# Kernel tuning notes

Hardware: AMD Instinct MI355X
Metric: run time of the kernel (lower is better)

## Reference

```python
import jax, jax.numpy as jnp
import numpy as np

INPUT, HIDDEN, OUTPUT = 512, 512, 512
B, S = 32, 2048


def setup_inputs() -> dict:
    key = jax.random.key(0)
    ks = jax.random.split(key, 8)
    s_in = 1.0 / np.sqrt(INPUT)
    s_h = 1.0 / np.sqrt(HIDDEN)
    return {
        "x": jax.random.normal(ks[0], (B, S, INPUT), dtype=jnp.float32),
        "W_xh": jax.random.uniform(ks[1], (HIDDEN, INPUT), jnp.float32, -s_in, s_in),
        "b_xh": jax.random.uniform(ks[2], (HIDDEN,), jnp.float32, -s_in, s_in),
        "W_hh": jax.random.uniform(ks[3], (HIDDEN, HIDDEN), jnp.float32, -s_h, s_h),
        "b_hh": jax.random.uniform(ks[4], (HIDDEN,), jnp.float32, -s_h, s_h),
        "b_h": jnp.zeros((HIDDEN,), jnp.float32),
        "W_fc": jax.random.uniform(ks[5], (OUTPUT, HIDDEN), jnp.float32, -s_h, s_h),
        "b_fc": jax.random.uniform(ks[6], (OUTPUT,), jnp.float32, -s_h, s_h),
    }


def reference(x, W_xh, b_xh, W_hh, b_hh, b_h, W_fc, b_fc):
    # Precompute the input projection for all timesteps in one big GEMM:
    # [B,S,I] @ [I,H] -> [B,S,H]; bias terms folded in once.
    xproj = jnp.einsum("bsi,hi->bsh", x, W_xh) + (b_xh + b_hh + b_h)
    h0 = jnp.zeros((x.shape[0], W_hh.shape[0]), x.dtype)

    def step(h, xp_t):
        h = jnp.tanh(xp_t + h @ W_hh.T)
        return h, None

    # scan over time: xproj transposed to [S,B,H]
    h_final, _ = jax.lax.scan(step, h0, jnp.swapaxes(xproj, 0, 1))
    return h_final @ W_fc.T + b_fc
```

## Files before the change

### kernel.cpp

```cpp
#include <hip/hip_runtime.h>

typedef _Float16 f16;
typedef _Float16 f16x8 __attribute__((ext_vector_type(8)));
typedef float    f32x4 __attribute__((ext_vector_type(4)));

#define NSTEP 2048
#define HID   512
#define BATCH 32
#define SEQL  2048

__global__ __launch_bounds__(256, 4) void wcvt_kernel(
    const float* __restrict__ W, f16* __restrict__ Wf)
{
    int i = (blockIdx.x * 256 + threadIdx.x) * 8;
    float4 a0 = *(const float4*)(W + i);
    float4 a1 = *(const float4*)(W + i + 4);
    f16x8 h;
    h[0] = (f16)a0.x; h[1] = (f16)a0.y; h[2] = (f16)a0.z; h[3] = (f16)a0.w;
    h[4] = (f16)a1.x; h[5] = (f16)a1.y; h[6] = (f16)a1.z; h[7] = (f16)a1.w;
    *(f16x8*)&Wf[i] = h;
}

#define P1_AS 40

__global__ __launch_bounds__(256, 2) void xproj_f16_kernel(
    const float* __restrict__ x, const f16* __restrict__ Wf16,
    const float* __restrict__ bxh, const float* __restrict__ bhh,
    const float* __restrict__ bh, f16* __restrict__ xp)
{
    __shared__ __align__(16) f16 As[64 * P1_AS];
    __shared__ __align__(16) f16 Bs[512 * P1_AS];

    const int t = threadIdx.x;
    const int wave = t >> 6, lane = t & 63;
    const size_t mbase = (size_t)blockIdx.x * 64;

    f32x4 acc[4][8];
#pragma unroll
    for (int i = 0; i < 4; i++)
#pragma unroll
        for (int j = 0; j < 8; j++) acc[i][j] = (f32x4){0.f, 0.f, 0.f, 0.f};

    const int r_st = t >> 2;
    const int koff = (t & 3) * 8;

    for (int k0 = 0; k0 < 512; k0 += 32) {
        __syncthreads();
        {
            const float* src = x + (mbase + r_st) * 512 + k0 + koff;
            float4 a0 = *(const float4*)src;
            float4 a1 = *(const float4*)(src + 4);
            f16x8 h;
            h[0] = (f16)a0.x; h[1] = (f16)a0.y; h[2] = (f16)a0.z; h[3] = (f16)a0.w;
            h[4] = (f16)a1.x; h[5] = (f16)a1.y; h[6] = (f16)a1.z; h[7] = (f16)a1.w;
            *(f16x8*)&As[r_st * P1_AS + koff] = h;
        }
#pragma unroll
        for (int i = 0; i < 8; i++) {
            int n = r_st + i * 64;
            *(f16x8*)&Bs[n * P1_AS + koff] =
                *(const f16x8*)(Wf16 + (size_t)n * 512 + k0 + koff);
        }
        __syncthreads();

        f16x8 af[4];
#pragma unroll
        for (int rt = 0; rt < 4; rt++)
            af[rt] = *(const f16x8*)&As[(rt * 16 + (lane & 15)) * P1_AS + (lane >> 4) * 8];
#pragma unroll
        for (int ct = 0; ct < 8; ct++) {
            f16x8 bf = *(const f16x8*)&Bs[((wave * 8 + ct) * 16 + (lane & 15)) * P1_AS + (lane >> 4) * 8];
#pragma unroll
            for (int rt = 0; rt < 4; rt++)
                acc[rt][ct] = __builtin_amdgcn_mfma_f32_16x16x32_f16(af[rt], bf, acc[rt][ct], 0, 0, 0);
        }
    }

#pragma unroll
    for (int ct = 0; ct < 8; ct++) {
        int n = wave * 128 + ct * 16 + (lane & 15);
        float bias = bxh[n] + bhh[n] + bh[n];
#pragma unroll
        for (int rt = 0; rt < 4; rt++) {
#pragma unroll
            for (int r = 0; r < 4; r++) {
                size_t m = mbase + rt * 16 + (lane >> 4) * 4 + r;
                xp[m * 512 + n] = (f16)(acc[rt][ct][r] + bias);
            }
        }
    }
}

__global__ __launch_bounds__(256, 2) void xproj_kernel(
    const float* __restrict__ x, const float* __restrict__ Wxh,
    const float* __restrict__ bxh, const float* __restrict__ bhh,
    const float* __restrict__ bh, f16* __restrict__ xp)
{
    __shared__ __align__(16) f16 As[64 * P1_AS];
    __shared__ __align__(16) f16 Bs[512 * P1_AS];

    const int t = threadIdx.x;
    const int wave = t >> 6, lane = t & 63;
    const size_t mbase = (size_t)blockIdx.x * 64;

    f32x4 acc[4][8];
#pragma unroll
    for (int i = 0; i < 4; i++)
#pragma unroll
        for (int j = 0; j < 8; j++) acc[i][j] = (f32x4){0.f, 0.f, 0.f, 0.f};

    const int r_st = t >> 2;
    const int koff = (t & 3) * 8;

    for (int k0 = 0; k0 < 512; k0 += 32) {
        __syncthreads();
        {
            const float* src = x + (mbase + r_st) * 512 + k0 + koff;
            float4 a0 = *(const float4*)src;
            float4 a1 = *(const float4*)(src + 4);
            f16x8 h;
            h[0] = (f16)a0.x; h[1] = (f16)a0.y; h[2] = (f16)a0.z; h[3] = (f16)a0.w;
            h[4] = (f16)a1.x; h[5] = (f16)a1.y; h[6] = (f16)a1.z; h[7] = (f16)a1.w;
            *(f16x8*)&As[r_st * P1_AS + koff] = h;
        }
#pragma unroll
        for (int i = 0; i < 8; i++) {
            int n = r_st + i * 64;
            const float* src = Wxh + (size_t)n * 512 + k0 + koff;
            float4 b0 = *(const float4*)src;
            float4 b1 = *(const float4*)(src + 4);
            f16x8 h;
            h[0] = (f16)b0.x; h[1] = (f16)b0.y; h[2] = (f16)b0.z; h[3] = (f16)b0.w;
            h[4] = (f16)b1.x; h[5] = (f16)b1.y; h[6] = (f16)b1.z; h[7] = (f16)b1.w;
            *(f16x8*)&Bs[n * P1_AS + koff] = h;
        }
        __syncthreads();

        f16x8 af[4];
#pragma unroll
        for (int rt = 0; rt < 4; rt++)
            af[rt] = *(const f16x8*)&As[(rt * 16 + (lane & 15)) * P1_AS + (lane >> 4) * 8];
#pragma unroll
        for (int ct = 0; ct < 8; ct++) {
            f16x8 bf = *(const f16x8*)&Bs[((wave * 8 + ct) * 16 + (lane & 15)) * P1_AS + (lane >> 4) * 8];
#pragma unroll
            for (int rt = 0; rt < 4; rt++)
                acc[rt][ct] = __builtin_amdgcn_mfma_f32_16x16x32_f16(af[rt], bf, acc[rt][ct], 0, 0, 0);
        }
    }

#pragma unroll
    for (int ct = 0; ct < 8; ct++) {
        int n = wave * 128 + ct * 16 + (lane & 15);
        float bias = bxh[n] + bhh[n] + bh[n];
#pragma unroll
        for (int rt = 0; rt < 4; rt++) {
#pragma unroll
            for (int r = 0; r < 4; r++) {
                size_t m = mbase + rt * 16 + (lane >> 4) * 4 + r;
                xp[m * 512 + n] = (f16)(acc[rt][ct][r] + bias);
            }
        }
    }
}

#define P2_LDS_BYTES (2 * HID * 2 + 8 * 16 * 64 * 16)

__global__ __launch_bounds__(512, 2) void rnn_kernel(
    const float* __restrict__ Whh, const f16* __restrict__ xp,
    f16* __restrict__ hfin)
{
    extern __shared__ __align__(16) char smem[];
    f16* hbuf0 = (f16*)smem;
    f16* hbuf1 = hbuf0 + HID;
    f16* ldsB  = hbuf1 + HID;

    const int t = threadIdx.x;
    const int wave = t >> 6, lane = t & 63;
    const int b = blockIdx.x;

    const int c_in = lane & 15;
    const int k8   = (lane >> 4) * 8;

    f16x8 wreg[48];
#pragma unroll
    for (int r = 0; r < 3; r++) {
        const float* wrow = Whh + (size_t)((wave * 4 + r) * 16 + c_in) * 512;
#pragma unroll
        for (int kf = 0; kf < 16; kf++) {
            float4 w0 = *(const float4*)(wrow + kf * 32 + k8);
            float4 w1 = *(const float4*)(wrow + kf * 32 + k8 + 4);
            f16x8 h;
            h[0] = (f16)w0.x; h[1] = (f16)w0.y; h[2] = (f16)w0.z; h[3] = (f16)w0.w;
            h[4] = (f16)w1.x; h[5] = (f16)w1.y; h[6] = (f16)w1.z; h[7] = (f16)w1.w;
            wreg[r * 16 + kf] = h;
        }
    }
    {
        const float* wrow = Whh + (size_t)((wave * 4 + 3) * 16 + c_in) * 512;
#pragma unroll
        for (int kf = 0; kf < 16; kf++) {
            float4 w0 = *(const float4*)(wrow + kf * 32 + k8);
            float4 w1 = *(const float4*)(wrow + kf * 32 + k8 + 4);
            f16x8 h;
            h[0] = (f16)w0.x; h[1] = (f16)w0.y; h[2] = (f16)w0.z; h[3] = (f16)w0.w;
            h[4] = (f16)w1.x; h[5] = (f16)w1.y; h[6] = (f16)w1.z; h[7] = (f16)w1.w;
            *(f16x8*)&ldsB[(size_t)wave * 8192 + kf * 512 + lane * 8] = h;
        }
    }
    hbuf0[t & (HID - 1)] = (f16)0.f;
    __syncthreads();

    const f16* xprow = xp + (size_t)b * SEQL * 512 + wave * 64 + lane;
    const int ldsb_base = wave * 8192 + lane * 8;

    float xv = (float)xprow[0];
    for (int s = 0; s < NSTEP; s++) {
        const f16* cur = (s & 1) ? hbuf1 : hbuf0;
        f16*       nxt = (s & 1) ? hbuf0 : hbuf1;
        int sn = (s + 1 < NSTEP) ? s + 1 : s;
        float xv_next = (float)xprow[(size_t)sn * 512];

        f32x4 a0 = (f32x4){0.f,0.f,0.f,0.f}, a1 = a0, a2 = a0, a3 = a0;
#pragma unroll
        for (int kf = 0; kf < 16; kf++) {
            f16x8 av = *(const f16x8*)&cur[kf * 32 + k8];
            a0 = __builtin_amdgcn_mfma_f32_16x16x32_f16(av, wreg[kf],      a0, 0, 0, 0);
            a1 = __builtin_amdgcn_mfma_f32_16x16x32_f16(av, wreg[16 + kf], a1, 0, 0, 0);
            a2 = __builtin_amdgcn_mfma_f32_16x16x32_f16(av, wreg[32 + kf], a2, 0, 0, 0);
            f16x8 bl = *(const f16x8*)&ldsB[ldsb_base + kf * 512];
            a3 = __builtin_amdgcn_mfma_f32_16x16x32_f16(av, bl, a3, 0, 0, 0);
        }
        int r = lane >> 4;
        float v = (r == 0) ? a0[0] : (r == 1) ? a1[0] : (r == 2) ? a2[0] : a3[0];
        v += xv;
        float e = __expf(2.f * v);
        v = 1.f - 2.f / (e + 1.f);
        nxt[wave * 64 + lane] = (f16)v;
        xv = xv_next;
        __syncthreads();
    }
    hfin[(size_t)b * 512 + t] = hbuf0[t & (HID - 1)];
}

#define P3_HS 520

__global__ __launch_bounds__(256, 2) void fc_kernel(
    const f16* __restrict__ hfin, const float* __restrict__ Wfc,
    const float* __restrict__ bfc, float* __restrict__ out)
{
    __shared__ __align__(16) f16 hs[BATCH * P3_HS];
    const int t = threadIdx.x;
    for (int i = 0; i < 64; i++) {
        int e = i * 256 + t;
        hs[(e >> 9) * P3_HS + (e & 511)] = hfin[e];
    }
    __syncthreads();

    const int bidx = t & 31;
    const int oi = t >> 5;
    const int o0 = blockIdx.x * 16;
    const int oA = o0 + oi, oB = o0 + oi + 8;
    const float* wA = Wfc + (size_t)oA * 512;
    const float* wB = Wfc + (size_t)oB * 512;

    float sA = 0.f, sB = 0.f;
#pragma unroll 4
    for (int kb = 0; kb < 64; kb++) {
        f16x8 hv = *(const f16x8*)&hs[bidx * P3_HS + kb * 8];
        float4 wa0 = *(const float4*)(wA + kb * 8);
        float4 wa1 = *(const float4*)(wA + kb * 8 + 4);
        float4 wb0 = *(const float4*)(wB + kb * 8);
        float4 wb1 = *(const float4*)(wB + kb * 8 + 4);
        float h0 = (float)hv[0], h1 = (float)hv[1], h2 = (float)hv[2], h3 = (float)hv[3];
        float h4 = (float)hv[4], h5 = (float)hv[5], h6 = (float)hv[6], h7 = (float)hv[7];
        sA += wa0.x*h0 + wa0.y*h1 + wa0.z*h2 + wa0.w*h3 + wa1.x*h4 + wa1.y*h5 + wa1.z*h6 + wa1.w*h7;
        sB += wb0.x*h0 + wb0.y*h1 + wb0.z*h2 + wb0.w*h3 + wb1.x*h4 + wb1.y*h5 + wb1.z*h6 + wb1.w*h7;
    }
    out[(size_t)bidx * 512 + oA] = sA + bfc[oA];
    out[(size_t)bidx * 512 + oB] = sB + bfc[oB];
}

extern "C" void kernel_launch(void* const* d_in, const int* in_sizes, int n_in,
                              void* d_out, int out_size, void* d_ws, size_t ws_size,
                              hipStream_t stream) {
    const float* x    = (const float*)d_in[0];
    const float* Wxh  = (const float*)d_in[1];
    const float* bxh  = (const float*)d_in[2];
    const float* Whh  = (const float*)d_in[3];
    const float* bhh  = (const float*)d_in[4];
    const float* bh   = (const float*)d_in[5];
    const float* Wfc  = (const float*)d_in[6];
    const float* bfc  = (const float*)d_in[7];
    float* outp = (float*)d_out;

    const size_t xp_bytes   = (size_t)BATCH * SEQL * 512 * 2;
    const size_t hfin_bytes = (size_t)BATCH * 512 * 2;
    f16* xp   = (f16*)d_ws;
    f16* hfin = (f16*)((char*)d_ws + xp_bytes);
    f16* wf16 = (f16*)((char*)d_ws + xp_bytes + hfin_bytes);

    hipFuncSetAttribute((const void*)rnn_kernel,
                        hipFuncAttributeMaxDynamicSharedMemorySize, 160 * 1024);

    if (ws_size >= xp_bytes + hfin_bytes + (size_t)512 * 512 * 2) {
        wcvt_kernel<<<128, 256, 0, stream>>>(Wxh, wf16);
        xproj_f16_kernel<<<(BATCH * SEQL) / 64, 256, 0, stream>>>(
            x, wf16, bxh, bhh, bh, xp);
    } else {
        xproj_kernel<<<(BATCH * SEQL) / 64, 256, 0, stream>>>(
            x, Wxh, bxh, bhh, bh, xp);
    }
    rnn_kernel<<<BATCH, 512, P2_LDS_BYTES, stream>>>(Whh, xp, hfin);
    fc_kernel<<<32, 256, 0, stream>>>(hfin, Wfc, bfc, outp);
}
```

Measured before the change: 2.685 ms.

## Split recurrence across cooperating blocks with global flag synchronization per timestep

Adds a recurrent kernel in which 8 blocks each own 64 hidden columns for the whole batch and keep their slice of W_hh in registers as f16. The hidden state is exchanged through a double-buffered global array. Each step waits on per-block release/acquire flags before reading the previous state. This replaces the per-batch-block design, which loads the full W_hh per block, with a batch-as-M MFMA layout, and it prefetches the next step's xproj values. The cost is a device-wide handshake through L2 on every one of the 2048 steps, and only 8 blocks are active. The weight-convert kernel now also zeroes the initial state and the flags.

```diff
diff --git a/kernel.cpp b/kernel.cpp
--- a/kernel.cpp
+++ b/kernel.cpp
@@ -8,17 +8,22 @@
 #define HID   512
 #define BATCH 32
 #define SEQL  2048
+#define NCOOP 8
 
 __global__ __launch_bounds__(256, 4) void wcvt_kernel(
-    const float* __restrict__ W, f16* __restrict__ Wf)
-{
-    int i = (blockIdx.x * 256 + threadIdx.x) * 8;
+    const float* __restrict__ W, f16* __restrict__ Wf,
+    unsigned int* __restrict__ hz, unsigned int* __restrict__ fz)
+{
+    int gid = blockIdx.x * 256 + threadIdx.x;
+    int i = gid * 8;
     float4 a0 = *(const float4*)(W + i);
     float4 a1 = *(const float4*)(W + i + 4);
     f16x8 h;
     h[0] = (f16)a0.x; h[1] = (f16)a0.y; h[2] = (f16)a0.z; h[3] = (f16)a0.w;
     h[4] = (f16)a1.x; h[5] = (f16)a1.y; h[6] = (f16)a1.z; h[7] = (f16)a1.w;
     *(f16x8*)&Wf[i] = h;
+    if (gid < 8192)      hz[gid] = 0u;
+    else if (gid < 8320) fz[gid - 8192] = 0u;
 }
 
 #define P1_AS 40
@@ -98,20 +103,16 @@
 {
     __shared__ __align__(16) f16 As[64 * P1_AS];
     __shared__ __align__(16) f16 Bs[512 * P1_AS];
-
     const int t = threadIdx.x;
     const int wave = t >> 6, lane = t & 63;
     const size_t mbase = (size_t)blockIdx.x * 64;
-
     f32x4 acc[4][8];
 #pragma unroll
     for (int i = 0; i < 4; i++)
 #pragma unroll
         for (int j = 0; j < 8; j++) acc[i][j] = (f32x4){0.f, 0.f, 0.f, 0.f};
-
     const int r_st = t >> 2;
     const int koff = (t & 3) * 8;
-
     for (int k0 = 0; k0 < 512; k0 += 32) {
         __syncthreads();
         {
@@ -135,7 +136,6 @@
             *(f16x8*)&Bs[n * P1_AS + koff] = h;
         }
         __syncthreads();
-
         f16x8 af[4];
 #pragma unroll
         for (int rt = 0; rt < 4; rt++)
@@ -148,7 +148,6 @@
                 acc[rt][ct] = __builtin_amdgcn_mfma_f32_16x16x32_f16(af[rt], bf, acc[rt][ct], 0, 0, 0);
         }
     }
-
 #pragma unroll
     for (int ct = 0; ct < 8; ct++) {
         int n = wave * 128 + ct * 16 + (lane & 15);
@@ -164,6 +163,104 @@
     }
 }
 
+__global__ __launch_bounds__(256, 1) void rnn_coop_kernel(
+    const float* __restrict__ Whh, const f16* __restrict__ xp,
+    f16* __restrict__ hstate, unsigned int* __restrict__ flags)
+{
+    const int t = threadIdx.x;
+    const int w = t >> 6, l = t & 63;
+    const int g = blockIdx.x;
+    const int Mt = w & 1;
+    const int p  = w >> 1;
+    const int c16 = l & 15;
+    const int k8  = (l >> 4) * 8;
+    const int rbase = (l >> 4) * 4;
+
+    const int col0 = g * 64 + p * 32 + c16;
+
+    f16x8 wb[2][16];
+#pragma unroll
+    for (int cti = 0; cti < 2; cti++) {
+        const float* wrow = Whh + (size_t)(col0 + cti * 16) * 512;
+#pragma unroll
+        for (int kf = 0; kf < 16; kf++) {
+            float4 w0 = *(const float4*)(wrow + kf * 32 + k8);
+            float4 w1 = *(const float4*)(wrow + kf * 32 + k8 + 4);
+            f16x8 h;
+            h[0] = (f16)w0.x; h[1] = (f16)w0.y; h[2] = (f16)w0.z; h[3] = (f16)w0.w;
+            h[4] = (f16)w1.x; h[5] = (f16)w1.y; h[6] = (f16)w1.z; h[7] = (f16)w1.w;
+            wb[cti][kf] = h;
+        }
+    }
+
+    f16* hs0 = hstate;
+    f16* hs1 = hstate + BATCH * HID;
+
+    float xc[2][4];
+#pragma unroll
+    for (int cti = 0; cti < 2; cti++)
+#pragma unroll
+        for (int r = 0; r < 4; r++)
+            xc[cti][r] = (float)xp[((size_t)(Mt * 16 + rbase + r) * SEQL) * 512
+                                   + col0 + cti * 16];
+
+    for (int s = 0; s < NSTEP; s++) {
+        const f16* hcur = (s & 1) ? hs1 : hs0;
+        f16*       hnxt = (s & 1) ? hs0 : hs1;
+
+        if (s > 0) {
+            if (t < NCOOP) {
+                while (__hip_atomic_load(&flags[t * 16], __ATOMIC_ACQUIRE,
+                                         __HIP_MEMORY_SCOPE_AGENT) < (unsigned)s)
+                    __builtin_amdgcn_s_sleep(1);
+            }
+            __syncthreads();
+            asm volatile("" ::: "memory");
+        }
+
+        int sn = (s + 1 < NSTEP) ? s + 1 : s;
+        float xn[2][4];
+#pragma unroll
+        for (int cti = 0; cti < 2; cti++)
+#pragma unroll
+            for (int r = 0; r < 4; r++)
+                xn[cti][r] = (float)xp[((size_t)(Mt * 16 + rbase + r) * SEQL + sn) * 512
+                                       + col0 + cti * 16];
+
+        f16x8 af[16];
+#pragma unroll
+        for (int kf = 0; kf < 16; kf++)
+            af[kf] = *(const f16x8*)&hcur[(Mt * 16 + c16) * HID + kf * 32 + k8];
+
+        f32x4 a0 = (f32x4){0.f, 0.f, 0.f, 0.f}, a1 = a0;
+#pragma unroll
+        for (int kf = 0; kf < 16; kf++) {
+            a0 = __builtin_amdgcn_mfma_f32_16x16x32_f16(af[kf], wb[0][kf], a0, 0, 0, 0);
+            a1 = __builtin_amdgcn_mfma_f32_16x16x32_f16(af[kf], wb[1][kf], a1, 0, 0, 0);
+        }
+
+#pragma unroll
+        for (int r = 0; r < 4; r++) {
+            int batch = Mt * 16 + rbase + r;
+            float v0 = a0[r] + xc[0][r];
+            float v1 = a1[r] + xc[1][r];
+            v0 = 1.f - 2.f / (__expf(2.f * v0) + 1.f);
+            v1 = 1.f - 2.f / (__expf(2.f * v1) + 1.f);
+            hnxt[batch * HID + col0]      = (f16)v0;
+            hnxt[batch * HID + col0 + 16] = (f16)v1;
+        }
+#pragma unroll
+        for (int cti = 0; cti < 2; cti++)
+#pragma unroll
+            for (int r = 0; r < 4; r++) xc[cti][r] = xn[cti][r];
+
+        __syncthreads();
+        if (t == 0)
+            __hip_atomic_store(&flags[g * 16], (unsigned)(s + 1),
+                               __ATOMIC_RELEASE, __HIP_MEMORY_SCOPE_AGENT);
+    }
+}
+
 #define P2_LDS_BYTES (2 * HID * 2 + 8 * 16 * 64 * 16)
 
 __global__ __launch_bounds__(512, 2) void rnn_kernel(
@@ -178,7 +275,6 @@
     const int t = threadIdx.x;
     const int wave = t >> 6, lane = t & 63;
     const int b = blockIdx.x;
-
     const int c_in = lane & 15;
     const int k8   = (lane >> 4) * 8;
 
@@ -294,23 +390,29 @@
     const float* bfc  = (const float*)d_in[7];
     float* outp = (float*)d_out;
 
-    const size_t xp_bytes   = (size_t)BATCH * SEQL * 512 * 2;
-    const size_t hfin_bytes = (size_t)BATCH * 512 * 2;
-    f16* xp   = (f16*)d_ws;
-    f16* hfin = (f16*)((char*)d_ws + xp_bytes);
-    f16* wf16 = (f16*)((char*)d_ws + xp_bytes + hfin_bytes);
-
-    hipFuncSetAttribute((const void*)rnn_kernel,
-                        hipFuncAttributeMaxDynamicSharedMemorySize, 160 * 1024);
-
-    if (ws_size >= xp_bytes + hfin_bytes + (size_t)512 * 512 * 2) {
-        wcvt_kernel<<<128, 256, 0, stream>>>(Wxh, wf16);
+    const size_t xp_bytes     = (size_t)BATCH * SEQL * 512 * 2;
+    const size_t wf16_bytes   = (size_t)512 * 512 * 2;
+    const size_t hstate_bytes = (size_t)2 * BATCH * HID * 2;
+    const size_t flags_bytes  = 4096;
+
+    f16* xp      = (f16*)d_ws;
+    f16* wf16    = (f16*)((char*)d_ws + xp_bytes);
+    f16* hstate  = (f16*)((char*)d_ws + xp_bytes + wf16_bytes);
+    unsigned int* flags = (unsigned int*)((char*)d_ws + xp_bytes + wf16_bytes + hstate_bytes);
+
+    if (ws_size >= xp_bytes + wf16_bytes + hstate_bytes + flags_bytes) {
+        wcvt_kernel<<<128, 256, 0, stream>>>(Wxh, wf16, (unsigned int*)hstate, flags);
         xproj_f16_kernel<<<(BATCH * SEQL) / 64, 256, 0, stream>>>(
             x, wf16, bxh, bhh, bh, xp);
+        rnn_coop_kernel<<<NCOOP, 256, 0, stream>>>(Whh, xp, hstate, flags);
+        fc_kernel<<<32, 256, 0, stream>>>(hstate , Wfc, bfc, outp);
     } else {
+        f16* hfin = (f16*)((char*)d_ws + xp_bytes);
+        hipFuncSetAttribute((const void*)rnn_kernel,
+                            hipFuncAttributeMaxDynamicSharedMemorySize, 160 * 1024);
         xproj_kernel<<<(BATCH * SEQL) / 64, 256, 0, stream>>>(
             x, Wxh, bxh, bhh, bh, xp);
-    }
-    rnn_kernel<<<BATCH, 512, P2_LDS_BYTES, stream>>>(Whh, xp, hfin);
-    fc_kernel<<<32, 256, 0, stream>>>(hfin, Wfc, bfc, outp);
-}
+        rnn_kernel<<<BATCH, 512, P2_LDS_BYTES, stream>>>(Whh, xp, hfin);
+        fc_kernel<<<32, 256, 0, stream>>>(hfin, Wfc, bfc, outp);
+    }
+}
```

After: 9.050 ms. 3.37x slower.

## Retile input-projection GEMM to 128x128 blocks with double-buffered LDS prefetch

Applied to the files above, without the earlier changes.

Replaces the 64x512-tile xproj kernel with one that tiles 128 rows by 128 columns per block. It stores operands in LDS in an MFMA-fragment-ready layout and double-buffers the K chunks, so global loads for the next chunk overlap the current MFMAs and only one barrier is needed per iteration. This targets the projection phase's LDS footprint and load stalls, at the cost of reading each x tile four times, once per N-block. The RNN recurrence, which likely dominates total time, is unchanged apart from a helper refactor.

```diff
diff --git a/kernel.cpp b/kernel.cpp
--- a/kernel.cpp
+++ b/kernel.cpp
@@ -9,119 +9,139 @@
 #define BATCH 32
 #define SEQL  2048
 
+static __device__ __forceinline__ f16x8 cvt8(float4 a, float4 b) {
+    f16x8 h;
+    h[0] = (f16)a.x; h[1] = (f16)a.y; h[2] = (f16)a.z; h[3] = (f16)a.w;
+    h[4] = (f16)b.x; h[5] = (f16)b.y; h[6] = (f16)b.z; h[7] = (f16)b.w;
+    return h;
+}
+
 __global__ __launch_bounds__(256, 4) void wcvt_kernel(
     const float* __restrict__ W, f16* __restrict__ Wf)
 {
     int i = (blockIdx.x * 256 + threadIdx.x) * 8;
     float4 a0 = *(const float4*)(W + i);
     float4 a1 = *(const float4*)(W + i + 4);
-    f16x8 h;
-    h[0] = (f16)a0.x; h[1] = (f16)a0.y; h[2] = (f16)a0.z; h[3] = (f16)a0.w;
-    h[4] = (f16)a1.x; h[5] = (f16)a1.y; h[6] = (f16)a1.z; h[7] = (f16)a1.w;
-    *(f16x8*)&Wf[i] = h;
-}
-
-#define P1_AS 40
-
-__global__ __launch_bounds__(256, 2) void xproj_f16_kernel(
+    *(f16x8*)&Wf[i] = cvt8(a0, a1);
+}
+
+__global__ __launch_bounds__(256, 2) void xproj_v3_kernel(
     const float* __restrict__ x, const f16* __restrict__ Wf16,
     const float* __restrict__ bxh, const float* __restrict__ bhh,
     const float* __restrict__ bh, f16* __restrict__ xp)
 {
+    __shared__ __align__(16) f16 Af[2][8 * 64 * 8];
+    __shared__ __align__(16) f16 Bf[2][8 * 64 * 8];
+
+    const int t = threadIdx.x;
+    const int wave = t >> 6, lane = t & 63;
+    const size_t mbase = (size_t)(blockIdx.x >> 2) * 128;
+    const int nbase = (blockIdx.x & 3) * 128;
+
+    const int r_st = t >> 1;
+    const int hh   = t & 1;
+    const int dq0  = (r_st >> 4) * 64 + (2 * hh) * 16 + (r_st & 15);
+    const int dq1  = dq0 + 16;
+
+    f32x4 acc[2][8];
+#pragma unroll
+    for (int i = 0; i < 2; i++)
+#pragma unroll
+        for (int j = 0; j < 8; j++) acc[i][j] = (f32x4){0.f, 0.f, 0.f, 0.f};
+
+    {
+        const float* asrc = x + (mbase + r_st) * 512 + hh * 16;
+        float4 a0 = *(const float4*)asrc;
+        float4 a1 = *(const float4*)(asrc + 4);
+        float4 a2 = *(const float4*)(asrc + 8);
+        float4 a3 = *(const float4*)(asrc + 12);
+        const f16* bsrc = Wf16 + (size_t)(nbase + r_st) * 512 + hh * 16;
+        f16x8 hb0 = *(const f16x8*)bsrc;
+        f16x8 hb1 = *(const f16x8*)(bsrc + 8);
+        *(f16x8*)&Af[0][dq0 * 8] = cvt8(a0, a1);
+        *(f16x8*)&Af[0][dq1 * 8] = cvt8(a2, a3);
+        *(f16x8*)&Bf[0][dq0 * 8] = hb0;
+        *(f16x8*)&Bf[0][dq1 * 8] = hb1;
+    }
+    __syncthreads();
+
+    int buf = 0;
+    for (int kc = 0; kc < 16; kc++) {
+        const int nb = buf ^ 1;
+        float4 a0, a1, a2, a3;
+        f16x8 hb0, hb1;
+        if (kc < 15) {
+            const int kn = (kc + 1) * 32;
+            const float* asrc = x + (mbase + r_st) * 512 + kn + hh * 16;
+            a0 = *(const float4*)asrc;
+            a1 = *(const float4*)(asrc + 4);
+            a2 = *(const float4*)(asrc + 8);
+            a3 = *(const float4*)(asrc + 12);
+            const f16* bsrc = Wf16 + (size_t)(nbase + r_st) * 512 + kn + hh * 16;
+            hb0 = *(const f16x8*)bsrc;
+            hb1 = *(const f16x8*)(bsrc + 8);
+        }
+
+        f16x8 af0 = *(const f16x8*)&Af[buf][((2 * wave + 0) * 64 + lane) * 8];
+        f16x8 af1 = *(const f16x8*)&Af[buf][((2 * wave + 1) * 64 + lane) * 8];
+#pragma unroll
+        for (int ct = 0; ct < 8; ct++) {
+            f16x8 bf = *(const f16x8*)&Bf[buf][(ct * 64 + lane) * 8];
+            acc[0][ct] = __builtin_amdgcn_mfma_f32_16x16x32_f16(af0, bf, acc[0][ct], 0, 0, 0);
+            acc[1][ct] = __builtin_amdgcn_mfma_f32_16x16x32_f16(af1, bf, acc[1][ct], 0, 0, 0);
+        }
+
+        if (kc < 15) {
+            *(f16x8*)&Af[nb][dq0 * 8] = cvt8(a0, a1);
+            *(f16x8*)&Af[nb][dq1 * 8] = cvt8(a2, a3);
+            *(f16x8*)&Bf[nb][dq0 * 8] = hb0;
+            *(f16x8*)&Bf[nb][dq1 * 8] = hb1;
+        }
+        __syncthreads();
+        buf = nb;
+    }
+
+#pragma unroll
+    for (int ct = 0; ct < 8; ct++) {
+        int n = nbase + ct * 16 + (lane & 15);
+        float bias = bxh[n] + bhh[n] + bh[n];
+#pragma unroll
+        for (int i = 0; i < 2; i++) {
+#pragma unroll
+            for (int r = 0; r < 4; r++) {
+                size_t m = mbase + (wave * 2 + i) * 16 + (lane >> 4) * 4 + r;
+                xp[m * 512 + n] = (f16)(acc[i][ct][r] + bias);
+            }
+        }
+    }
+}
+
+#define P1_AS 40
+
+__global__ __launch_bounds__(256, 2) void xproj_kernel(
+    const float* __restrict__ x, const float* __restrict__ Wxh,
+    const float* __restrict__ bxh, const float* __restrict__ bhh,
+    const float* __restrict__ bh, f16* __restrict__ xp)
+{
     __shared__ __align__(16) f16 As[64 * P1_AS];
     __shared__ __align__(16) f16 Bs[512 * P1_AS];
-
     const int t = threadIdx.x;
     const int wave = t >> 6, lane = t & 63;
     const size_t mbase = (size_t)blockIdx.x * 64;
-
     f32x4 acc[4][8];
 #pragma unroll
     for (int i = 0; i < 4; i++)
 #pragma unroll
         for (int j = 0; j < 8; j++) acc[i][j] = (f32x4){0.f, 0.f, 0.f, 0.f};
-
     const int r_st = t >> 2;
     const int koff = (t & 3) * 8;
-
     for (int k0 = 0; k0 < 512; k0 += 32) {
         __syncthreads();
         {
             const float* src = x + (mbase + r_st) * 512 + k0 + koff;
             float4 a0 = *(const float4*)src;
             float4 a1 = *(const float4*)(src + 4);
-            f16x8 h;
-            h[0] = (f16)a0.x; h[1] = (f16)a0.y; h[2] = (f16)a0.z; h[3] = (f16)a0.w;
-            h[4] = (f16)a1.x; h[5] = (f16)a1.y; h[6] = (f16)a1.z; h[7] = (f16)a1.w;
-            *(f16x8*)&As[r_st * P1_AS + koff] = h;
-        }
-#pragma unroll
-        for (int i = 0; i < 8; i++) {
-            int n = r_st + i * 64;
-            *(f16x8*)&Bs[n * P1_AS + koff] =
-                *(const f16x8*)(Wf16 + (size_t)n * 512 + k0 + koff);
-        }
-        __syncthreads();
-
-        f16x8 af[4];
-#pragma unroll
-        for (int rt = 0; rt < 4; rt++)
-            af[rt] = *(const f16x8*)&As[(rt * 16 + (lane & 15)) * P1_AS + (lane >> 4) * 8];
-#pragma unroll
-        for (int ct = 0; ct < 8; ct++) {
-            f16x8 bf = *(const f16x8*)&Bs[((wave * 8 + ct) * 16 + (lane & 15)) * P1_AS + (lane >> 4) * 8];
-#pragma unroll
-            for (int rt = 0; rt < 4; rt++)
-                acc[rt][ct] = __builtin_amdgcn_mfma_f32_16x16x32_f16(af[rt], bf, acc[rt][ct], 0, 0, 0);
-        }
-    }
-
-#pragma unroll
-    for (int ct = 0; ct < 8; ct++) {
-        int n = wave * 128 + ct * 16 + (lane & 15);
-        float bias = bxh[n] + bhh[n] + bh[n];
-#pragma unroll
-        for (int rt = 0; rt < 4; rt++) {
-#pragma unroll
-            for (int r = 0; r < 4; r++) {
-                size_t m = mbase + rt * 16 + (lane >> 4) * 4 + r;
-                xp[m * 512 + n] = (f16)(acc[rt][ct][r] + bias);
-            }
-        }
-    }
-}
-
-__global__ __launch_bounds__(256, 2) void xproj_kernel(
-    const float* __restrict__ x, const float* __restrict__ Wxh,
-    const float* __restrict__ bxh, const float* __restrict__ bhh,
-    const float* __restrict__ bh, f16* __restrict__ xp)
-{
-    __shared__ __align__(16) f16 As[64 * P1_AS];
-    __shared__ __align__(16) f16 Bs[512 * P1_AS];
-
-    const int t = threadIdx.x;
-    const int wave = t >> 6, lane = t & 63;
-    const size_t mbase = (size_t)blockIdx.x * 64;
-
-    f32x4 acc[4][8];
-#pragma unroll
-    for (int i = 0; i < 4; i++)
-#pragma unroll
-        for (int j = 0; j < 8; j++) acc[i][j] = (f32x4){0.f, 0.f, 0.f, 0.f};
-
-    const int r_st = t >> 2;
-    const int koff = (t & 3) * 8;
-
-    for (int k0 = 0; k0 < 512; k0 += 32) {
-        __syncthreads();
-        {
-            const float* src = x + (mbase + r_st) * 512 + k0 + koff;
-            float4 a0 = *(const float4*)src;
-            float4 a1 = *(const float4*)(src + 4);
-            f16x8 h;
-            h[0] = (f16)a0.x; h[1] = (f16)a0.y; h[2] = (f16)a0.z; h[3] = (f16)a0.w;
-            h[4] = (f16)a1.x; h[5] = (f16)a1.y; h[6] = (f16)a1.z; h[7] = (f16)a1.w;
-            *(f16x8*)&As[r_st * P1_AS + koff] = h;
+            *(f16x8*)&As[r_st * P1_AS + koff] = cvt8(a0, a1);
         }
 #pragma unroll
         for (int i = 0; i < 8; i++) {
@@ -129,13 +149,9 @@
             const float* src = Wxh + (size_t)n * 512 + k0 + koff;
             float4 b0 = *(const float4*)src;
             float4 b1 = *(const float4*)(src + 4);
-            f16x8 h;
-            h[0] = (f16)b0.x; h[1] = (f16)b0.y; h[2] = (f16)b0.z; h[3] = (f16)b0.w;
-            h[4] = (f16)b1.x; h[5] = (f16)b1.y; h[6] = (f16)b1.z; h[7] = (f16)b1.w;
-            *(f16x8*)&Bs[n * P1_AS + koff] = h;
+            *(f16x8*)&Bs[n * P1_AS + koff] = cvt8(b0, b1);
         }
         __syncthreads();
-
         f16x8 af[4];
 #pragma unroll
         for (int rt = 0; rt < 4; rt++)
@@ -148,7 +164,6 @@
                 acc[rt][ct] = __builtin_amdgcn_mfma_f32_16x16x32_f16(af[rt], bf, acc[rt][ct], 0, 0, 0);
         }
     }
-
 #pragma unroll
     for (int ct = 0; ct < 8; ct++) {
         int n = wave * 128 + ct * 16 + (lane & 15);
@@ -178,7 +193,6 @@
     const int t = threadIdx.x;
     const int wave = t >> 6, lane = t & 63;
     const int b = blockIdx.x;
-
     const int c_in = lane & 15;
     const int k8   = (lane >> 4) * 8;
 
@@ -190,10 +204,7 @@
         for (int kf = 0; kf < 16; kf++) {
             float4 w0 = *(const float4*)(wrow + kf * 32 + k8);
             float4 w1 = *(const float4*)(wrow + kf * 32 + k8 + 4);
-            f16x8 h;
-            h[0] = (f16)w0.x; h[1] = (f16)w0.y; h[2] = (f16)w0.z; h[3] = (f16)w0.w;
-            h[4] = (f16)w1.x; h[5] = (f16)w1.y; h[6] = (f16)w1.z; h[7] = (f16)w1.w;
-            wreg[r * 16 + kf] = h;
+            wreg[r * 16 + kf] = cvt8(w0, w1);
         }
     }
     {
@@ -202,10 +213,7 @@
         for (int kf = 0; kf < 16; kf++) {
             float4 w0 = *(const float4*)(wrow + kf * 32 + k8);
             float4 w1 = *(const float4*)(wrow + kf * 32 + k8 + 4);
-            f16x8 h;
-            h[0] = (f16)w0.x; h[1] = (f16)w0.y; h[2] = (f16)w0.z; h[3] = (f16)w0.w;
-            h[4] = (f16)w1.x; h[5] = (f16)w1.y; h[6] = (f16)w1.z; h[7] = (f16)w1.w;
-            *(f16x8*)&ldsB[(size_t)wave * 8192 + kf * 512 + lane * 8] = h;
+            *(f16x8*)&ldsB[(size_t)wave * 8192 + kf * 512 + lane * 8] = cvt8(w0, w1);
         }
     }
     hbuf0[t & (HID - 1)] = (f16)0.f;
@@ -296,6 +304,8 @@
 
     const size_t xp_bytes   = (size_t)BATCH * SEQL * 512 * 2;
     const size_t hfin_bytes = (size_t)BATCH * 512 * 2;
+    const size_t wf16_bytes = (size_t)512 * 512 * 2;
+
     f16* xp   = (f16*)d_ws;
     f16* hfin = (f16*)((char*)d_ws + xp_bytes);
     f16* wf16 = (f16*)((char*)d_ws + xp_bytes + hfin_bytes);
@@ -303,9 +313,9 @@
     hipFuncSetAttribute((const void*)rnn_kernel,
                         hipFuncAttributeMaxDynamicSharedMemorySize, 160 * 1024);
 
-    if (ws_size >= xp_bytes + hfin_bytes + (size_t)512 * 512 * 2) {
+    if (ws_size >= xp_bytes + hfin_bytes + wf16_bytes) {
         wcvt_kernel<<<128, 256, 0, stream>>>(Wxh, wf16);
-        xproj_f16_kernel<<<(BATCH * SEQL) / 64, 256, 0, stream>>>(
+        xproj_v3_kernel<<<(BATCH * SEQL / 128) * 4, 256, 0, stream>>>(
             x, wf16, bxh, bhh, bh, xp);
     } else {
         xproj_kernel<<<(BATCH * SEQL) / 64, 256, 0, stream>>>(
```

Result: no change. 2.703 ms (+0.7%).
